# Kernel tuning notes

Hardware: AMD Instinct MI355X
Metric: run time of the kernel (lower is better)

Reference implementation:

```python
import jax, jax.numpy as jnp
import numpy as np

N = 50000
E = 800000
IN_C = 128
OUT_C = 256
NUM_REL = 6


def _rgcn_conv(x, src, dst, etype, W, root, bias):
    # PyG RGCNConv (no bases, aggr='mean'):
    # out = x @ root + bias + sum_r mean_{j in N_r(i)}(x_j) @ W[r]
    n = x.shape[0]
    xe = x[src]  # [E, d_in] gather of source features
    out = x @ root + bias
    for r in range(NUM_REL):
        m = (etype == r)
        s = jax.ops.segment_sum(jnp.where(m[:, None], xe, 0.0), dst, num_segments=n)
        c = jax.ops.segment_sum(m.astype(x.dtype), dst, num_segments=n)
        out = out + (s / jnp.maximum(c, 1.0)[:, None]) @ W[r]
    return out


def setup_inputs() -> dict:
    key = jax.random.key(0)
    ks = jax.random.split(key, 16)
    half = OUT_C // 2

    def g(k, shape, fan_in):
        return jax.random.normal(k, shape, dtype=jnp.float32) / np.sqrt(fan_in)

    return {
        "x": jax.random.normal(ks[0], (N, IN_C), dtype=jnp.float32),
        "edge_index": jax.random.randint(ks[1], (2, E), 0, N, dtype=jnp.int32),
        "edge_type": jax.random.randint(ks[2], (E,), 0, NUM_REL, dtype=jnp.int32),
        # encoder MLP
        "enc_w0": g(ks[3], (IN_C, OUT_C), IN_C), "enc_b0": jnp.zeros((OUT_C,), jnp.float32),
        "enc_w1": g(ks[4], (OUT_C, OUT_C), OUT_C), "enc_b1": jnp.zeros((OUT_C,), jnp.float32),
        "enc_w2": g(ks[5], (OUT_C, half), OUT_C), "enc_b2": jnp.zeros((half,), jnp.float32),
        # conv1
        "W1": g(ks[6], (NUM_REL, IN_C, OUT_C), IN_C), "root1": g(ks[7], (IN_C, OUT_C), IN_C),
        "b1": jnp.zeros((OUT_C,), jnp.float32),
        # conv2
        "W2": g(ks[8], (NUM_REL, OUT_C, OUT_C), OUT_C), "root2": g(ks[9], (OUT_C, OUT_C), OUT_C),
        "b2": jnp.zeros((OUT_C,), jnp.float32),
        # conv_out
        "W3": g(ks[10], (NUM_REL, OUT_C, half), OUT_C), "root3": g(ks[11], (OUT_C, half), OUT_C),
        "b3": jnp.zeros((half,), jnp.float32),
    }


def reference(x, edge_index, edge_type,
              enc_w0, enc_b0, enc_w1, enc_b1, enc_w2, enc_b2,
              W1, root1, b1, W2, root2, b2, W3, root3, b3):
    src, dst = edge_index[0], edge_index[1]
    # dense encoder branch
    h = jax.nn.relu(x @ enc_w0 + enc_b0)
    h = jax.nn.relu(h @ enc_w1 + enc_b1)
    self_feat = h @ enc_w2 + enc_b2
    # RGCN branch
    g1 = jax.nn.relu(_rgcn_conv(x, src, dst, edge_type, W1, root1, b1))
    g2 = jax.nn.relu(_rgcn_conv(g1, src, dst, edge_type, W2, root2, b2))
    graph_feat = _rgcn_conv(g2, src, dst, edge_type, W3, root3, b3)
    return jnp.concatenate([self_feat, graph_feat], axis=-1)
```

## Files before the change

kernel.cpp:

```cpp
#include <hip/hip_runtime.h>

#define NN   50000
#define EE   800000
#define INC  128
#define OUTC 256
#define HALF 128
#define NREL 6
#define NCELL (NN * NREL)
#define NPAD 50048

typedef __attribute__((ext_vector_type(4))) short s16x4;
typedef __attribute__((ext_vector_type(8))) short bf16x8;
typedef __attribute__((ext_vector_type(4))) float f32x4;

__device__ __forceinline__ float b2f(short b) {
    unsigned u = ((unsigned)(unsigned short)b) << 16;
    return __uint_as_float(u);
}
__device__ __forceinline__ short f2b(float f) {
    unsigned u = __float_as_uint(f);
    unsigned r = (u + 0x7fffu + ((u >> 16) & 1u)) >> 16;
    return (short)r;
}

__device__ __forceinline__ void gload16(const void* g, void* l) {
    __builtin_amdgcn_global_load_lds(
        (const __attribute__((address_space(1))) void*)g,
        (__attribute__((address_space(3))) void*)l, 16, 0, 0);
}

__global__ __launch_bounds__(256) void count_k(const int* __restrict__ dst,
                                               const int* __restrict__ et,
                                               int* __restrict__ cnt) {
    int e = blockIdx.x * 256 + threadIdx.x;
    if (e < EE) atomicAdd(&cnt[dst[e] * NREL + et[e]], 1);
}

__global__ __launch_bounds__(256) void scanA_k(const int* __restrict__ cnt,
                                               int* __restrict__ off,
                                               int* __restrict__ bsum, int n) {
    __shared__ int sh[256];
    int t = threadIdx.x;
    int base = blockIdx.x * 512 + t * 2;
    int v0 = (base < n) ? cnt[base] : 0;
    int v1 = (base + 1 < n) ? cnt[base + 1] : 0;
    int s = v0 + v1;
    sh[t] = s; __syncthreads();
    for (int o = 1; o < 256; o <<= 1) {
        int u = (t >= o) ? sh[t - o] : 0;
        __syncthreads();
        sh[t] += u;
        __syncthreads();
    }
    int excl = sh[t] - s;
    if (base < n)     off[base]     = excl;
    if (base + 1 < n) off[base + 1] = excl + v0;
    if (t == 255) bsum[blockIdx.x] = sh[255];
}

__global__ __launch_bounds__(1024) void scanB_k(int* __restrict__ bsum, int nb) {
    __shared__ int sh[1024];
    int t = threadIdx.x;
    int s = (t < nb) ? bsum[t] : 0;
    sh[t] = s; __syncthreads();
    for (int o = 1; o < 1024; o <<= 1) {
        int u = (t >= o) ? sh[t - o] : 0;
        __syncthreads();
        sh[t] += u;
        __syncthreads();
    }
    if (t < nb) bsum[t] = sh[t] - s;
}

__global__ __launch_bounds__(256) void scanC_k(int* __restrict__ off,
                                               const int* __restrict__ bsum, int n) {
    int i = blockIdx.x * 256 + threadIdx.x;
    if (i < n) off[i] += bsum[i >> 9];
    if (i == 0) off[n] = EE;
}

__global__ __launch_bounds__(256) void copyint_k(const int* __restrict__ a,
                                                 int* __restrict__ b, int n) {
    int i = blockIdx.x * 256 + threadIdx.x;
    if (i < n) b[i] = a[i];
}

__global__ __launch_bounds__(256) void fill_k(const int* __restrict__ src,
                                              const int* __restrict__ dst,
                                              const int* __restrict__ et,
                                              int* __restrict__ cur,
                                              int* __restrict__ es) {
    int e = blockIdx.x * 256 + threadIdx.x;
    if (e < EE) {
        int key = dst[e] * NREL + et[e];
        int p = atomicAdd(&cur[key], 1);
        es[p] = src[e];
    }
}

__global__ __launch_bounds__(256) void cast_x_k(const float* __restrict__ x,
                                                short* __restrict__ xb, int n4) {
    int i = blockIdx.x * 256 + threadIdx.x;
    if (i < n4) {
        float4 v = ((const float4*)x)[i];
        s16x4 o;
        o[0] = f2b(v.x); o[1] = f2b(v.y); o[2] = f2b(v.z); o[3] = f2b(v.w);
        ((s16x4*)xb)[i] = o;
    }
}

__global__ __launch_bounds__(256) void wtcat2_k(const float* __restrict__ root,
                                                const float* __restrict__ W,
                                                int K, int D, int Ncols,
                                                short* __restrict__ BT) {
    int i = blockIdx.x * 256 + threadIdx.x;
    if (i >= Ncols * K) return;
    int n = i / K, k = i - n * K;
    float v;
    if (n < D) {
        v = root[(size_t)k * D + n];
    } else {
        int nn = n - D;
        int r = nn / D, c = nn - r * D;
        v = W[((size_t)r * K + k) * D + c];
    }
    BT[(size_t)n * K + k] = f2b(v);
}

#define ACH(R, q) ((((R) << 2) | ((q) ^ ((R) & 3) ^ (((R) >> 2) & 1))) * 8)

__global__ __launch_bounds__(256) void gemm2_k(
    const short* __restrict__ A1, const short* __restrict__ B1,
    const float* __restrict__ bias1, int relu1,
    short* __restrict__ Cb1, int ldcb1, float* __restrict__ Cf1, int ldcf1,
    const short* __restrict__ A2, const short* __restrict__ B2,
    const float* __restrict__ bias2, int relu2,
    short* __restrict__ Cb2, int ldcb2, float* __restrict__ Cf2, int ldcf2,
    int M, int K, int nby1) {
    __shared__ __align__(16) char smem[16384];
    short* As = (short*)smem;
    short* Bs = As + 128 * 32;
    const int tid = threadIdx.x;
    const int wave = tid >> 6, lane = tid & 63;
    const int wm = (wave & 1) * 64, wn = (wave >> 1) * 64;
    const int l16 = lane & 15, quad = lane >> 4;
    const int bm = blockIdx.x * 128;

    const short* A; const short* BT; const float* bias;
    int relu; short* Cb; int ldcb; float* Cf; int ldcf; int bn;
    if ((int)blockIdx.y < nby1) {
        A = A1; BT = B1; bias = bias1; relu = relu1;
        Cb = Cb1; ldcb = ldcb1; Cf = Cf1; ldcf = ldcf1;
        bn = blockIdx.y * 128;
    } else {
        A = A2; BT = B2; bias = bias2; relu = relu2;
        Cb = Cb2; ldcb = ldcb2; Cf = Cf2; ldcf = ldcf2;
        bn = (blockIdx.y - nby1) * 128;
    }

    const int s0 = tid, s1 = tid + 256;
    const int r0 = s0 >> 2, c0 = (s0 & 3) ^ (r0 & 3) ^ ((r0 >> 2) & 1);
    const int r1 = s1 >> 2, c1 = (s1 & 3) ^ (r1 & 3) ^ ((r1 >> 2) & 1);

    f32x4 acc[4][4];
    #pragma unroll
    for (int i = 0; i < 4; ++i)
        #pragma unroll
        for (int j = 0; j < 4; ++j)
            acc[i][j] = (f32x4)0.f;

    for (int k0 = 0; k0 < K; k0 += 32) {
        gload16(A + (size_t)(bm + r0) * K + k0 + c0 * 8, As + (wave * 64) * 8);
        gload16(A + (size_t)(bm + r1) * K + k0 + c1 * 8, As + (256 + wave * 64) * 8);
        gload16(BT + (size_t)(bn + r0) * K + k0 + c0 * 8, Bs + (wave * 64) * 8);
        gload16(BT + (size_t)(bn + r1) * K + k0 + c1 * 8, Bs + (256 + wave * 64) * 8);
        __syncthreads();
        bf16x8 af[4], bf[4];
        #pragma unroll
        for (int mt = 0; mt < 4; ++mt)
            af[mt] = *(const bf16x8*)&As[ACH(wm + mt * 16 + l16, quad)];
        #pragma unroll
        for (int nt = 0; nt < 4; ++nt)
            bf[nt] = *(const bf16x8*)&Bs[ACH(wn + nt * 16 + l16, quad)];
        #pragma unroll
        for (int mt = 0; mt < 4; ++mt)
            #pragma unroll
            for (int nt = 0; nt < 4; ++nt)
                acc[mt][nt] = __builtin_amdgcn_mfma_f32_16x16x32_bf16(
                    af[mt], bf[nt], acc[mt][nt], 0, 0, 0);
        __syncthreads();
    }

    float bv[4];
    #pragma unroll
    for (int nt = 0; nt < 4; ++nt)
        bv[nt] = bias ? bias[bn + wn + nt * 16 + l16] : 0.f;

    if (Cb) {
        short* Es = (short*)smem;
        #pragma unroll
        for (int mt = 0; mt < 4; ++mt) {
            __syncthreads();
            int srb = (wave & 1) * 16 + quad * 4;
            #pragma unroll
            for (int nt = 0; nt < 4; ++nt) {
                int sc = wn + nt * 16 + l16;
                #pragma unroll
                for (int r = 0; r < 4; ++r) {
                    float v = acc[mt][nt][r] + bv[nt];
                    if (relu) v = fmaxf(v, 0.f);
                    Es[(srb + r) * 128 + sc] = f2b(v);
                }
            }
            __syncthreads();
            #pragma unroll
            for (int h = 0; h < 2; ++h) {
                int c = tid + h * 256;
                int rr = c >> 4, cc = c & 15;
                int grow = bm + (rr >> 4) * 64 + mt * 16 + (rr & 15);
                if (grow < M)
                    *(bf16x8*)(Cb + (size_t)grow * ldcb + bn + cc * 8) =
                        *(const bf16x8*)&Es[rr * 128 + cc * 8];
            }
        }
    } else {
        float* Ef = (float*)smem;
        #pragma unroll
        for (int mt = 0; mt < 4; ++mt) {
            __syncthreads();
            int srb = (wave & 1) * 16 + quad * 4;
            #pragma unroll
            for (int nt = 0; nt < 4; ++nt) {
                int sc = wn + nt * 16 + l16;
                #pragma unroll
                for (int r = 0; r < 4; ++r) {
                    float v = acc[mt][nt][r] + bv[nt];
                    if (relu) v = fmaxf(v, 0.f);
                    Ef[(srb + r) * 128 + sc] = v;
                }
            }
            __syncthreads();
            #pragma unroll
            for (int h = 0; h < 4; ++h) {
                int c = tid + h * 256;
                int rr = c >> 5, cc = c & 31;
                int grow = bm + (rr >> 4) * 64 + mt * 16 + (rr & 15);
                if (grow < M)
                    *(float4*)(Cf + (size_t)grow * ldcf + bn + cc * 4) =
                        *(const float4*)&Ef[rr * 128 + cc * 4];
            }
        }
    }
}

template<int D>
__global__ __launch_bounds__(256) void gagg_k(
    const short* __restrict__ H, int ldh,
    int rfirst, int rlast, int colbase, int self0,
    const int* __restrict__ off, const int* __restrict__ es,
    const float* __restrict__ accin,
    const float* __restrict__ bias, int relu,
    short* __restrict__ Ob, float* __restrict__ Of, int ldo) {
    constexpr int LPN = D / 4;
    constexpr int NPB = 256 / LPN;
    int sub = threadIdx.x / LPN, lane = threadIdx.x % LPN;
    int node = blockIdx.x * NPB + sub;
    if (node >= NN) return;
    int c0 = lane * 4;

    float a0, a1, a2, a3;
    if (accin) {
        float4 t = *(const float4*)(accin + (size_t)node * D + c0);
        a0 = t.x; a1 = t.y; a2 = t.z; a3 = t.w;
    } else {
        a0 = a1 = a2 = a3 = 0.f;
    }
    if (self0) {
        s16x4 v = *(const s16x4*)(H + (size_t)node * ldh + c0);
        a0 += b2f(v[0]); a1 += b2f(v[1]); a2 += b2f(v[2]); a3 += b2f(v[3]);
    }
    int cell0 = node * NREL;
    for (int r = rfirst; r < rlast; ++r) {
        int beg = off[cell0 + r], end = off[cell0 + r + 1];
        if (end == beg) continue;
        int colo = (colbase + r) * D + c0;
        float s0 = 0.f, s1 = 0.f, s2 = 0.f, s3 = 0.f;
        int j = beg;
        for (; j + 3 < end; j += 4) {
            s16x4 v0 = *(const s16x4*)(H + (size_t)es[j] * ldh + colo);
            s16x4 v1 = *(const s16x4*)(H + (size_t)es[j + 1] * ldh + colo);
            s16x4 v2 = *(const s16x4*)(H + (size_t)es[j + 2] * ldh + colo);
            s16x4 v3 = *(const s16x4*)(H + (size_t)es[j + 3] * ldh + colo);
            s0 += b2f(v0[0]) + b2f(v1[0]) + b2f(v2[0]) + b2f(v3[0]);
            s1 += b2f(v0[1]) + b2f(v1[1]) + b2f(v2[1]) + b2f(v3[1]);
            s2 += b2f(v0[2]) + b2f(v1[2]) + b2f(v2[2]) + b2f(v3[2]);
            s3 += b2f(v0[3]) + b2f(v1[3]) + b2f(v2[3]) + b2f(v3[3]);
        }
        for (; j < end; ++j) {
            s16x4 v = *(const s16x4*)(H + (size_t)es[j] * ldh + colo);
            s0 += b2f(v[0]); s1 += b2f(v[1]); s2 += b2f(v[2]); s3 += b2f(v[3]);
        }
        float inv = 1.f / (float)(end - beg);
        a0 += s0 * inv; a1 += s1 * inv; a2 += s2 * inv; a3 += s3 * inv;
    }
    if (bias) {
        float4 bv = *(const float4*)(bias + c0);
        a0 += bv.x; a1 += bv.y; a2 += bv.z; a3 += bv.w;
    }
    if (relu) {
        a0 = fmaxf(a0, 0.f); a1 = fmaxf(a1, 0.f);
        a2 = fmaxf(a2, 0.f); a3 = fmaxf(a3, 0.f);
    }
    if (Ob) {
        s16x4 o;
        o[0] = f2b(a0); o[1] = f2b(a1); o[2] = f2b(a2); o[3] = f2b(a3);
        *(s16x4*)(Ob + (size_t)node * ldo + c0) = o;
    } else {
        float4 o; o.x = a0; o.y = a1; o.z = a2; o.w = a3;
        *(float4*)(Of + (size_t)node * ldo + c0) = o;
    }
}

extern "C" void kernel_launch(void* const* d_in, const int* in_sizes, int n_in,
                              void* d_out, int out_size, void* d_ws, size_t ws_size,
                              hipStream_t stream) {
    const float* x      = (const float*)d_in[0];
    const int*   ei     = (const int*)d_in[1];
    const int*   srcv   = ei;
    const int*   dstv   = ei + EE;
    const int*   et     = (const int*)d_in[2];
    const float* enc_w0 = (const float*)d_in[3];
    const float* enc_b0 = (const float*)d_in[4];
    const float* enc_w1 = (const float*)d_in[5];
    const float* enc_b1 = (const float*)d_in[6];
    const float* enc_w2 = (const float*)d_in[7];
    const float* enc_b2 = (const float*)d_in[8];
    const float* W1     = (const float*)d_in[9];
    const float* root1  = (const float*)d_in[10];
    const float* b1     = (const float*)d_in[11];
    const float* W2     = (const float*)d_in[12];
    const float* root2  = (const float*)d_in[13];
    const float* b2     = (const float*)d_in[14];
    const float* W3     = (const float*)d_in[15];
    const float* root3  = (const float*)d_in[16];
    const float* b3     = (const float*)d_in[17];
    float* out = (float*)d_out;

    char* p = (char*)d_ws;
    auto alloc = [&](size_t bytes) -> char* {
        char* r = p; p += (bytes + 255) & ~(size_t)255; return r;
    };
    short* xb  = (short*)alloc((size_t)NPAD * INC * 2);
    short* g1  = (short*)alloc((size_t)NPAD * OUTC * 2);
    short* g2  = (short*)alloc((size_t)NPAD * OUTC * 2);
    short* BT1 = (short*)alloc((size_t)1792 * INC * 2);
    short* BT2 = (short*)alloc((size_t)1792 * OUTC * 2);
    short* BT3 = (short*)alloc((size_t)896 * OUTC * 2);
    short* ET0 = (short*)alloc((size_t)OUTC * INC * 2);
    short* ET1 = (short*)alloc((size_t)OUTC * OUTC * 2);
    short* ET2 = (short*)alloc((size_t)HALF * OUTC * 2);
    int* CNT  = (int*)alloc((size_t)NCELL * 4);
    int* OFF  = (int*)alloc((size_t)(NCELL + 1) * 4);
    int* CUR  = (int*)alloc((size_t)NCELL * 4);
    int* ES   = (int*)alloc((size_t)EE * 4);
    int* BSUM = (int*)alloc(1024 * 4);
    size_t fixed = (size_t)(p - (char*)d_ws);

    const size_t Hfull = (size_t)NPAD * 1792 * 2;
    const size_t Esz   = (size_t)NPAD * OUTC * 2;
    bool tierA = fixed + Hfull + 2 * Esz + 1024 <= ws_size;
    bool fullH = tierA || (fixed + Hfull + 1024 <= ws_size);
    short* H = (short*)alloc(fullH ? Hfull : (size_t)NPAD * 1024 * 2);
    short* e1 = nullptr; short* e2 = nullptr; float* ACC = nullptr;
    if (tierA) { e1 = (short*)alloc(Esz); e2 = (short*)alloc(Esz); }
    if (!fullH) ACC = (float*)alloc((size_t)NPAD * OUTC * 4);

    hipMemsetAsync(CNT, 0, (size_t)NCELL * 4, stream);
    count_k<<<EE / 256, 256, 0, stream>>>(dstv, et, CNT);
    int nbA = (NCELL + 511) / 512;
    scanA_k<<<nbA, 256, 0, stream>>>(CNT, OFF, BSUM, NCELL);
    scanB_k<<<1, 1024, 0, stream>>>(BSUM, nbA);
    scanC_k<<<(NCELL + 255) / 256, 256, 0, stream>>>(OFF, BSUM, NCELL);
    copyint_k<<<(NCELL + 255) / 256, 256, 0, stream>>>(OFF, CUR, NCELL);
    fill_k<<<EE / 256, 256, 0, stream>>>(srcv, dstv, et, CUR, ES);

    cast_x_k<<<(NN * INC / 4 + 255) / 256, 256, 0, stream>>>(x, xb, NN * INC / 4);
    auto wt = [&](const float* root, const float* W, int K, int D, int Ncols, short* BT) {
        wtcat2_k<<<(Ncols * K + 255) / 256, 256, 0, stream>>>(root, W, K, D, Ncols, BT);
    };
    wt(root1, W1, INC, OUTC, 1792, BT1);
    wt(root2, W2, OUTC, OUTC, 1792, BT2);
    wt(root3, W3, OUTC, HALF, 896, BT3);
    wt(enc_w0, nullptr, INC, OUTC, OUTC, ET0);
    wt(enc_w1, nullptr, OUTC, OUTC, OUTC, ET1);
    wt(enc_w2, nullptr, OUTC, HALF, HALF, ET2);

    auto gemm1 = [&](const short* A, const short* BT, int M, int K, int Ncols,
                     const float* bias, int relu, short* Cb, int ldcb, float* Cf, int ldcf) {
        dim3 grid((M + 127) / 128, Ncols / 128);
        gemm2_k<<<grid, 256, 0, stream>>>(A, BT, bias, relu, Cb, ldcb, Cf, ldcf,
                                          A, BT, bias, relu, Cb, ldcb, Cf, ldcf,
                                          M, K, grid.y);
    };

    if (tierA) {
        gemm2_k<<<dim3(391, 16), 256, 0, stream>>>(
            xb, BT1, nullptr, 0, H, 1792, nullptr, 0,
            xb, ET0, enc_b0, 1, e1, OUTC, nullptr, 0,
            NN, INC, 14);
        gagg_k<256><<<12500, 256, 0, stream>>>(H, 1792, 0, NREL, 1, 1,
            OFF, ES, nullptr, b1, 1, g1, nullptr, OUTC);
        gemm2_k<<<dim3(391, 16), 256, 0, stream>>>(
            g1, BT2, nullptr, 0, H, 1792, nullptr, 0,
            e1, ET1, enc_b1, 1, e2, OUTC, nullptr, 0,
            NN, OUTC, 14);
        gagg_k<256><<<12500, 256, 0, stream>>>(H, 1792, 0, NREL, 1, 1,
            OFF, ES, nullptr, b2, 1, g2, nullptr, OUTC);
        gemm2_k<<<dim3(391, 8), 256, 0, stream>>>(
            g2, BT3, nullptr, 0, H, 896, nullptr, 0,
            e2, ET2, enc_b2, 0, nullptr, 0, out, OUTC,
            NN, OUTC, 7);
        gagg_k<128><<<6250, 256, 0, stream>>>(H, 896, 0, NREL, 1, 1,
            OFF, ES, nullptr, b3, 0, nullptr, out + HALF, OUTC);
        return;
    }

    gemm1(xb, ET0, NN, INC, OUTC, enc_b0, 1, g1, OUTC, nullptr, 0);
    gemm1(g1, ET1, NN, OUTC, OUTC, enc_b1, 1, g2, OUTC, nullptr, 0);
    gemm1(g2, ET2, NN, OUTC, HALF, enc_b2, 0, nullptr, 0, out, OUTC);

    auto conv = [&](const short* A, int K, int D, const short* BT,
                    const float* bias, int relu, short* Ob, float* Of) {
        int NPB = 256 / (D / 4);
        int gg = (NN + NPB - 1) / NPB;
        if (fullH) {
            gemm1(A, BT, NN, K, 7 * D, nullptr, 0, H, 7 * D, nullptr, 0);
            if (D == 256)
                gagg_k<256><<<gg, 256, 0, stream>>>(H, 7 * D, 0, NREL, 1, 1,
                    OFF, ES, nullptr, bias, relu, Ob, Of, OUTC);
            else
                gagg_k<128><<<gg, 256, 0, stream>>>(H, 7 * D, 0, NREL, 1, 1,
                    OFF, ES, nullptr, bias, relu, Ob, Of, OUTC);
        } else {
            gemm1(A, BT, NN, K, 4 * D, nullptr, 0, H, 4 * D, nullptr, 0);
            if (D == 256)
                gagg_k<256><<<gg, 256, 0, stream>>>(H, 4 * D, 0, 3, 1, 1,
                    OFF, ES, nullptr, nullptr, 0, nullptr, ACC, D);
            else
                gagg_k<128><<<gg, 256, 0, stream>>>(H, 4 * D, 0, 3, 1, 1,
                    OFF, ES, nullptr, nullptr, 0, nullptr, ACC, D);
            gemm1(A, BT + (size_t)4 * D * (size_t)K, NN, K, 3 * D, nullptr, 0, H, 3 * D, nullptr, 0);
            if (D == 256)
                gagg_k<256><<<gg, 256, 0, stream>>>(H, 3 * D, 3, NREL, -3, 0,
                    OFF, ES, ACC, bias, relu, Ob, Of, OUTC);
            else
                gagg_k<128><<<gg, 256, 0, stream>>>(H, 3 * D, 3, NREL, -3, 0,
                    OFF, ES, ACC, bias, relu, Ob, Of, OUTC);
        }
    };

    conv(xb, INC,  OUTC, BT1, b1, 1, g1, nullptr);
    conv(g1, OUTC, OUTC, BT2, b2, 1, g2, nullptr);
    conv(g2, OUTC, HALF, BT3, b3, 0, nullptr, out + HALF);
}
```

Before: 740.9 us.

## Flatten per-node edge aggregation with precomputed relation-tagged indices and mean weights

Adds a preprocessing kernel that writes each edge's source index tagged with its relation in the high bits, plus a per-edge 1/degree weight. A new aggregation kernel then walks all of a node's edges in one loop and does a weighted accumulate. This removes the per-relation loop, its short segments and the scalar tails, so more gathers can be in flight. It also changes the GEMM LDS staging offset from wave*64 to the per-thread slot index, and shortens the unroll of the old fallback aggregation kernel from 4 to 2. The cost is extra preprocessing work and two extra E-sized arrays that must be read during aggregation.

```diff
diff --git a/kernel.cpp b/kernel.cpp
--- a/kernel.cpp
+++ b/kernel.cpp
@@ -95,6 +95,22 @@
         int key = dst[e] * NREL + et[e];
         int p = atomicAdd(&cur[key], 1);
         es[p] = src[e];
+    }
+}
+
+__global__ __launch_bounds__(256) void wgt_k(const int* __restrict__ off,
+                                             const int* __restrict__ es,
+                                             int* __restrict__ ep,
+                                             float* __restrict__ wgt) {
+    int c = blockIdx.x * 256 + threadIdx.x;
+    if (c >= NCELL) return;
+    int beg = off[c], end = off[c + 1];
+    if (end <= beg) return;
+    float inv = 1.f / (float)(end - beg);
+    int rtag = (c % NREL) << 24;
+    for (int p = beg; p < end; ++p) {
+        ep[p] = es[p] | rtag;
+        wgt[p] = inv;
     }
 }
 
@@ -170,10 +186,10 @@
             acc[i][j] = (f32x4)0.f;
 
     for (int k0 = 0; k0 < K; k0 += 32) {
-        gload16(A + (size_t)(bm + r0) * K + k0 + c0 * 8, As + (wave * 64) * 8);
-        gload16(A + (size_t)(bm + r1) * K + k0 + c1 * 8, As + (256 + wave * 64) * 8);
-        gload16(BT + (size_t)(bn + r0) * K + k0 + c0 * 8, Bs + (wave * 64) * 8);
-        gload16(BT + (size_t)(bn + r1) * K + k0 + c1 * 8, Bs + (256 + wave * 64) * 8);
+        gload16(A + (size_t)(bm + r0) * K + k0 + c0 * 8, As + s0 * 8);
+        gload16(A + (size_t)(bm + r1) * K + k0 + c1 * 8, As + s1 * 8);
+        gload16(BT + (size_t)(bn + r0) * K + k0 + c0 * 8, Bs + s0 * 8);
+        gload16(BT + (size_t)(bn + r1) * K + k0 + c1 * 8, Bs + s1 * 8);
         __syncthreads();
         bf16x8 af[4], bf[4];
         #pragma unroll
@@ -254,6 +270,62 @@
 }
 
 template<int D>
+__global__ __launch_bounds__(256) void gagg2_k(
+    const short* __restrict__ H, int ldh,
+    const int* __restrict__ off,
+    const int* __restrict__ ep, const float* __restrict__ wgt,
+    const float* __restrict__ bias, int relu,
+    short* __restrict__ Ob, float* __restrict__ Of, int ldo) {
+    constexpr int LPN = D / 4;
+    constexpr int NPB = 256 / LPN;
+    int sub = threadIdx.x / LPN, lane = threadIdx.x % LPN;
+    int node = blockIdx.x * NPB + sub;
+    if (node >= NN) return;
+    int c0 = lane * 4;
+    const short* Hc = H + c0 + D;
+
+    s16x4 sv = *(const s16x4*)(H + (size_t)node * ldh + c0);
+    float a0 = b2f(sv[0]), a1 = b2f(sv[1]), a2 = b2f(sv[2]), a3 = b2f(sv[3]);
+
+    int jb = off[node * NREL], je = off[node * NREL + NREL];
+    int j = jb;
+    for (; j + 3 < je; j += 4) {
+        int u0 = ep[j], u1 = ep[j + 1], u2 = ep[j + 2], u3 = ep[j + 3];
+        float w0 = wgt[j], w1 = wgt[j + 1], w2 = wgt[j + 2], w3 = wgt[j + 3];
+        s16x4 x0 = *(const s16x4*)(Hc + (size_t)(u0 & 0xFFFFFF) * ldh + (u0 >> 24) * D);
+        s16x4 x1 = *(const s16x4*)(Hc + (size_t)(u1 & 0xFFFFFF) * ldh + (u1 >> 24) * D);
+        s16x4 x2 = *(const s16x4*)(Hc + (size_t)(u2 & 0xFFFFFF) * ldh + (u2 >> 24) * D);
+        s16x4 x3 = *(const s16x4*)(Hc + (size_t)(u3 & 0xFFFFFF) * ldh + (u3 >> 24) * D);
+        a0 += w0 * b2f(x0[0]) + w1 * b2f(x1[0]) + w2 * b2f(x2[0]) + w3 * b2f(x3[0]);
+        a1 += w0 * b2f(x0[1]) + w1 * b2f(x1[1]) + w2 * b2f(x2[1]) + w3 * b2f(x3[1]);
+        a2 += w0 * b2f(x0[2]) + w1 * b2f(x1[2]) + w2 * b2f(x2[2]) + w3 * b2f(x3[2]);
+        a3 += w0 * b2f(x0[3]) + w1 * b2f(x1[3]) + w2 * b2f(x2[3]) + w3 * b2f(x3[3]);
+    }
+    for (; j < je; ++j) {
+        int u = ep[j]; float w = wgt[j];
+        s16x4 x = *(const s16x4*)(Hc + (size_t)(u & 0xFFFFFF) * ldh + (u >> 24) * D);
+        a0 += w * b2f(x[0]); a1 += w * b2f(x[1]);
+        a2 += w * b2f(x[2]); a3 += w * b2f(x[3]);
+    }
+    if (bias) {
+        float4 bv = *(const float4*)(bias + c0);
+        a0 += bv.x; a1 += bv.y; a2 += bv.z; a3 += bv.w;
+    }
+    if (relu) {
+        a0 = fmaxf(a0, 0.f); a1 = fmaxf(a1, 0.f);
+        a2 = fmaxf(a2, 0.f); a3 = fmaxf(a3, 0.f);
+    }
+    if (Ob) {
+        s16x4 o;
+        o[0] = f2b(a0); o[1] = f2b(a1); o[2] = f2b(a2); o[3] = f2b(a3);
+        *(s16x4*)(Ob + (size_t)node * ldo + c0) = o;
+    } else {
+        float4 o; o.x = a0; o.y = a1; o.z = a2; o.w = a3;
+        *(float4*)(Of + (size_t)node * ldo + c0) = o;
+    }
+}
+
+template<int D>
 __global__ __launch_bounds__(256) void gagg_k(
     const short* __restrict__ H, int ldh,
     int rfirst, int rlast, int colbase, int self0,
@@ -286,17 +358,15 @@
         int colo = (colbase + r) * D + c0;
         float s0 = 0.f, s1 = 0.f, s2 = 0.f, s3 = 0.f;
         int j = beg;
-        for (; j + 3 < end; j += 4) {
-            s16x4 v0 = *(const s16x4*)(H + (size_t)es[j] * ldh + colo);
-            s16x4 v1 = *(const s16x4*)(H + (size_t)es[j + 1] * ldh + colo);
-            s16x4 v2 = *(const s16x4*)(H + (size_t)es[j + 2] * ldh + colo);
-            s16x4 v3 = *(const s16x4*)(H + (size_t)es[j + 3] * ldh + colo);
-            s0 += b2f(v0[0]) + b2f(v1[0]) + b2f(v2[0]) + b2f(v3[0]);
-            s1 += b2f(v0[1]) + b2f(v1[1]) + b2f(v2[1]) + b2f(v3[1]);
-            s2 += b2f(v0[2]) + b2f(v1[2]) + b2f(v2[2]) + b2f(v3[2]);
-            s3 += b2f(v0[3]) + b2f(v1[3]) + b2f(v2[3]) + b2f(v3[3]);
+        for (; j + 1 < end; j += 2) {
+            s16x4 v = *(const s16x4*)(H + (size_t)es[j] * ldh + colo);
+            s16x4 w = *(const s16x4*)(H + (size_t)es[j + 1] * ldh + colo);
+            s0 += b2f(v[0]) + b2f(w[0]);
+            s1 += b2f(v[1]) + b2f(w[1]);
+            s2 += b2f(v[2]) + b2f(w[2]);
+            s3 += b2f(v[3]) + b2f(w[3]);
         }
-        for (; j < end; ++j) {
+        if (j < end) {
             s16x4 v = *(const s16x4*)(H + (size_t)es[j] * ldh + colo);
             s0 += b2f(v[0]); s1 += b2f(v[1]); s2 += b2f(v[2]); s3 += b2f(v[3]);
         }
@@ -363,6 +433,8 @@
     int* OFF  = (int*)alloc((size_t)(NCELL + 1) * 4);
     int* CUR  = (int*)alloc((size_t)NCELL * 4);
     int* ES   = (int*)alloc((size_t)EE * 4);
+    int* EP   = (int*)alloc((size_t)EE * 4);
+    float* WG = (float*)alloc((size_t)EE * 4);
     int* BSUM = (int*)alloc(1024 * 4);
     size_t fixed = (size_t)(p - (char*)d_ws);
 
@@ -383,6 +455,7 @@
     scanC_k<<<(NCELL + 255) / 256, 256, 0, stream>>>(OFF, BSUM, NCELL);
     copyint_k<<<(NCELL + 255) / 256, 256, 0, stream>>>(OFF, CUR, NCELL);
     fill_k<<<EE / 256, 256, 0, stream>>>(srcv, dstv, et, CUR, ES);
+    wgt_k<<<(NCELL + 255) / 256, 256, 0, stream>>>(OFF, ES, EP, WG);
 
     cast_x_k<<<(NN * INC / 4 + 255) / 256, 256, 0, stream>>>(x, xb, NN * INC / 4);
     auto wt = [&](const float* root, const float* W, int K, int D, int Ncols, short* BT) {
@@ -408,20 +481,20 @@
             xb, BT1, nullptr, 0, H, 1792, nullptr, 0,
             xb, ET0, enc_b0, 1, e1, OUTC, nullptr, 0,
             NN, INC, 14);
-        gagg_k<256><<<12500, 256, 0, stream>>>(H, 1792, 0, NREL, 1, 1,
-            OFF, ES, nullptr, b1, 1, g1, nullptr, OUTC);
+        gagg2_k<256><<<12500, 256, 0, stream>>>(H, 1792, OFF, EP, WG,
+            b1, 1, g1, nullptr, OUTC);
         gemm2_k<<<dim3(391, 16), 256, 0, stream>>>(
             g1, BT2, nullptr, 0, H, 1792, nullptr, 0,
             e1, ET1, enc_b1, 1, e2, OUTC, nullptr, 0,
             NN, OUTC, 14);
-        gagg_k<256><<<12500, 256, 0, stream>>>(H, 1792, 0, NREL, 1, 1,
-            OFF, ES, nullptr, b2, 1, g2, nullptr, OUTC);
+        gagg2_k<256><<<12500, 256, 0, stream>>>(H, 1792, OFF, EP, WG,
+            b2, 1, g2, nullptr, OUTC);
         gemm2_k<<<dim3(391, 8), 256, 0, stream>>>(
             g2, BT3, nullptr, 0, H, 896, nullptr, 0,
             e2, ET2, enc_b2, 0, nullptr, 0, out, OUTC,
             NN, OUTC, 7);
-        gagg_k<128><<<6250, 256, 0, stream>>>(H, 896, 0, NREL, 1, 1,
-            OFF, ES, nullptr, b3, 0, nullptr, out + HALF, OUTC);
+        gagg2_k<128><<<6250, 256, 0, stream>>>(H, 896, OFF, EP, WG,
+            b3, 0, nullptr, out + HALF, OUTC);
         return;
     }
 
```

New measurement: 736.2 us. Within noise of the previous version (-0.6%).
